# Optimization experiments

Measured on AMD Instinct MI355X. Metric: run time of the kernel, lower is better.

## Reference

```python
import jax, jax.numpy as jnp
import numpy as np
import math

EPS = 1e-7
K_NEIGHBORS = 32  # matches init kwarg k

def _project(x, c):
    norm = jnp.linalg.norm(x, axis=-1, keepdims=True).clip(EPS)
    sqrt_c = jnp.sqrt(c).clip(EPS)
    max_norm = (1.0 - EPS) / sqrt_c
    return x * jnp.minimum(max_norm / norm, 1.0)

def _mobius_add(x, y, c):
    x2 = jnp.sum(x * x, axis=-1, keepdims=True)
    y2 = jnp.sum(y * y, axis=-1, keepdims=True)
    xy = jnp.sum(x * y, axis=-1, keepdims=True)
    num = (1 + 2 * c * xy + c * y2) * x + (1 - c * x2) * y
    den = 1 + 2 * c * xy + c * c * x2 * y2
    return _project(num / den.clip(EPS), c)

def _dist(x, y, c):
    sqrt_c = jnp.sqrt(c).clip(EPS)
    diff = _mobius_add(x, -y, c)
    dn = jnp.linalg.norm(diff, axis=-1)
    arg = jnp.minimum(sqrt_c * dn.clip(EPS, 1 - EPS), 1.0 - EPS)
    return 2.0 * jnp.arctanh(arg) / sqrt_c

def _logmap0(y, c):
    sqrt_c = jnp.sqrt(c).clip(EPS)
    yn = jnp.linalg.norm(y, axis=-1, keepdims=True)
    is_zero = yn < EPS
    syn = yn.clip(EPS)
    arg = jnp.minimum(sqrt_c * syn, 1.0 - EPS)
    mag = jnp.arctanh(arg) / sqrt_c
    return jnp.where(is_zero, jnp.zeros_like(y), mag * y / syn)

def _layernorm(x, g, b):
    m = x.mean(-1, keepdims=True)
    v = x.var(-1, keepdims=True)
    return (x - m) / jnp.sqrt(v + 1e-6) * g + b

def setup_inputs() -> dict:
    key = jax.random.key(0)
    B, N, D, P, H = 2, 2048, 512, 3, 8
    ks = jax.random.split(key, 16)
    s = 0.02
    d = {}
    d['x'] = jax.random.normal(ks[0], (B, N, D), dtype=jnp.float32)
    d['positions'] = jax.random.normal(ks[1], (B, N, P), dtype=jnp.float32) * 0.1
    d['c'] = jnp.float32(1.0)
    d['Wq'] = jax.random.normal(ks[2], (D, D), jnp.float32) * s; d['bq'] = jnp.zeros((D,), jnp.float32)
    d['Wk'] = jax.random.normal(ks[3], (D, D), jnp.float32) * s; d['bk'] = jnp.zeros((D,), jnp.float32)
    d['Wv'] = jax.random.normal(ks[4], (D, D), jnp.float32) * s; d['bv'] = jnp.zeros((D,), jnp.float32)
    d['Wg'] = jax.random.normal(ks[5], (P, D), jnp.float32) * s; d['bg'] = jnp.zeros((D,), jnp.float32)
    d['Wo'] = jax.random.normal(ks[6], (D, D), jnp.float32) * s; d['bo'] = jnp.zeros((D,), jnp.float32)
    d['Wf1'] = jax.random.normal(ks[7], (D, 4 * D), jnp.float32) * s; d['bf1'] = jnp.zeros((4 * D,), jnp.float32)
    d['Wf2'] = jax.random.normal(ks[8], (4 * D, D), jnp.float32) * s; d['bf2'] = jnp.zeros((D,), jnp.float32)
    d['g1'] = jnp.ones((D,), jnp.float32); d['b1'] = jnp.zeros((D,), jnp.float32)
    d['g2'] = jnp.ones((D,), jnp.float32); d['b2'] = jnp.zeros((D,), jnp.float32)
    d['ascale'] = jnp.ones((H,), jnp.float32)
    d['fscale'] = jnp.ones((H,), jnp.float32)
    return d

def reference(x, positions, c, Wq, bq, Wk, bk, Wv, bv, Wg, bg, Wo, bo, Wf1, bf1, Wf2, bf2, g1, b1, g2, b2, ascale, fscale):
    B, N, D = x.shape
    H = ascale.shape[0]
    hd = D // H
    K = K_NEIGHBORS

    xn = _layernorm(x, g1, b1)
    q = (xn @ Wq + bq).reshape(B, N, H, hd)
    k = (xn @ Wk + bk).reshape(B, N, H, hd)
    v = (xn @ Wv + bv).reshape(B, N, H, hd)

    # full pairwise hyperbolic distance matrix [B, N, N]
    dmat = _dist(positions[:, :, None, :], positions[:, None, :, :], c)
    idx = jax.lax.top_k(-dmat, K)[1]  # [B, N, K]

    bidx = jnp.arange(B)[:, None, None]
    key_pos = positions[bidx, idx]                 # [B, N, K, P]
    qpos = positions[:, :, None, :]                # [B, N, 1, P]
    geo = _logmap0(_mobius_add(-qpos, key_pos, c), c)
    geo_v = (geo @ Wg + bg).reshape(B, N, K, H, hd)

    kg = k[bidx, idx]                              # [B, N, K, H, hd]
    vg = v[bidx, idx]

    align = jnp.einsum('bnhd,bnkhd->bhnk', q, geo_v)
    feat = jnp.einsum('bnhd,bnkhd->bhnk', q, kg) / math.sqrt(hd)
    scores = fscale[None, :, None, None] * feat + ascale[None, :, None, None] * align
    w = jax.nn.softmax(scores.astype(jnp.float32), axis=-1)
    attn = jnp.einsum('bhnk,bnkhd->bnhd', w, vg).reshape(B, N, D)

    x1 = x + attn @ Wo + bo
    h = _layernorm(x1, g2, b2)
    x2 = x1 + jax.nn.gelu(h @ Wf1 + bf1) @ Wf2 + bf2
    return x2
```

## Files before the change

### kernel.cpp

```cpp
#include <hip/hip_runtime.h>
#include <math.h>

#define EPSF 1e-7f

constexpr int Bb = 2, Nn = 2048, Dd = 512, Hh = 8, HD = 64, KK = 32;
constexpr int ROWS = Bb * Nn;

typedef __attribute__((ext_vector_type(8))) short bf16x8;
typedef __attribute__((ext_vector_type(4))) float f32x4;
typedef __attribute__((ext_vector_type(8))) unsigned short u16x8;
typedef unsigned long long u64;

__device__ inline unsigned short f2bf(float f) {
    union { float f; unsigned int u; } v; v.f = f;
    unsigned int u = v.u;
    unsigned int r = (u + 0x7fffu + ((u >> 16) & 1u)) >> 16;
    return (unsigned short)r;
}

__device__ inline float bf2f(short s) {
    union { unsigned int u; float f; } x;
    x.u = ((unsigned int)(unsigned short)s) << 16;
    return x.f;
}

__device__ inline float gelu_tanh(float v) {
    float u = v + 0.044715f * v * v * v;
    return 0.5f * v * (1.f + tanhf(0.79788456080286535588f * u));
}

__device__ __forceinline__ void tcvt(float (*tile)[65], const float* __restrict__ in,
                                     unsigned short* __restrict__ out,
                                     int K, int N, int bx, int by) {
    int k0 = by * 64, n0 = bx * 64;
    int t = threadIdx.x;
    int lr = t >> 6, lc = t & 63;
#pragma unroll 4
    for (int p = 0; p < 16; ++p) {
        int r = p * 4 + lr;
        tile[r][lc] = in[(size_t)(k0 + r) * N + n0 + lc];
    }
    __syncthreads();
#pragma unroll 4
    for (int p = 0; p < 16; ++p) {
        int n = p * 4 + lr;
        out[(size_t)(n0 + n) * K + k0 + lc] = f2bf(tile[lc][n]);
    }
}

__device__ __forceinline__ void ln_row(const float* __restrict__ x,
                                       const float* __restrict__ g,
                                       const float* __restrict__ b,
                                       unsigned short* __restrict__ out,
                                       int row, int lane) {
    const float* xr = x + (size_t)row * Dd;
    float4 v0 = *(const float4*)(xr + lane * 8);
    float4 v1 = *(const float4*)(xr + lane * 8 + 4);
    float s = v0.x + v0.y + v0.z + v0.w + v1.x + v1.y + v1.z + v1.w;
    float s2 = v0.x * v0.x + v0.y * v0.y + v0.z * v0.z + v0.w * v0.w +
               v1.x * v1.x + v1.y * v1.y + v1.z * v1.z + v1.w * v1.w;
    for (int o = 32; o; o >>= 1) { s += __shfl_xor(s, o); s2 += __shfl_xor(s2, o); }
    float mean = s * (1.f / Dd);
    float var = s2 * (1.f / Dd) - mean * mean;
    float rstd = rsqrtf(var + 1e-6f);
    float4 g0 = *(const float4*)(g + lane * 8);
    float4 g1v = *(const float4*)(g + lane * 8 + 4);
    float4 b0 = *(const float4*)(b + lane * 8);
    float4 b1v = *(const float4*)(b + lane * 8 + 4);
    u16x8 o;
    o[0] = f2bf((v0.x - mean) * rstd * g0.x + b0.x);
    o[1] = f2bf((v0.y - mean) * rstd * g0.y + b0.y);
    o[2] = f2bf((v0.z - mean) * rstd * g0.z + b0.z);
    o[3] = f2bf((v0.w - mean) * rstd * g0.w + b0.w);
    o[4] = f2bf((v1.x - mean) * rstd * g1v.x + b1v.x);
    o[5] = f2bf((v1.y - mean) * rstd * g1v.y + b1v.y);
    o[6] = f2bf((v1.z - mean) * rstd * g1v.z + b1v.z);
    o[7] = f2bf((v1.w - mean) * rstd * g1v.w + b1v.w);
    *(u16x8*)(out + (size_t)row * Dd + lane * 8) = o;
}

__global__ __launch_bounds__(256) void ln_kernel(const float* __restrict__ x,
                                                 const float* __restrict__ g,
                                                 const float* __restrict__ b,
                                                 unsigned short* __restrict__ out) {
    ln_row(x, g, b, out, blockIdx.x * 4 + (threadIdx.x >> 6), threadIdx.x & 63);
}

template <int CTRL>
__device__ inline float dpp_f(float v) {
    int i = __float_as_int(v);
    i = __builtin_amdgcn_update_dpp(i, i, CTRL, 0xF, 0xF, false);
    return __int_as_float(i);
}
template <int CTRL>
__device__ inline unsigned dpp_u(unsigned v) {
    return (unsigned)__builtin_amdgcn_update_dpp((int)v, (int)v, CTRL, 0xF, 0xF, false);
}

__device__ inline float wave_min_f32(float v) {
    v = fminf(v, dpp_f<0xB1>(v));
    v = fminf(v, dpp_f<0x4E>(v));
    v = fminf(v, dpp_f<0x141>(v));
    v = fminf(v, dpp_f<0x140>(v));
    v = fminf(v, __shfl_xor(v, 16));
    v = fminf(v, __shfl_xor(v, 32));
    return v;
}
__device__ inline unsigned wave_min_u32(unsigned v) {
    unsigned o;
    o = dpp_u<0xB1>(v);  v = o < v ? o : v;
    o = dpp_u<0x4E>(v);  v = o < v ? o : v;
    o = dpp_u<0x141>(v); v = o < v ? o : v;
    o = dpp_u<0x140>(v); v = o < v ? o : v;
    o = __shfl_xor(v, 16); v = o < v ? o : v;
    o = __shfl_xor(v, 32); v = o < v ? o : v;
    return v;
}

__device__ __forceinline__ void topk_body(char* smem, const float* __restrict__ pos,
                                          const float* __restrict__ cp,
                                          int* __restrict__ idx_out, int bid) {
    float* s_px = (float*)smem;
    float* s_py = s_px + Nn;
    float* s_pz = s_py + Nn;
    float* s_u  = s_pz + Nn;
    int* s_out  = (int*)(s_u + Nn);
    int b = bid >> 9;
    int q0 = (bid & 511) * 4;
    int t = threadIdx.x;
    float c = *cp;
    const float* pb = pos + (size_t)b * Nn * 3;
    for (int j = t; j < Nn; j += 256) {
        float px = pb[j * 3 + 0], py = pb[j * 3 + 1], pz = pb[j * 3 + 2];
        s_px[j] = px; s_py[j] = py; s_pz[j] = pz;
        s_u[j] = c * (px * px + py * py + pz * pz);
    }
    __syncthreads();
    int wave = t >> 6, lane = t & 63;
    int n = q0 + wave;
    float qx = s_px[n], qy = s_py[n], qz = s_pz[n];
    float cx2 = s_u[n];
    float x2 = cx2 / c;
    float B = 1.f - cx2;
    float rc = 1.f / c;
    float B2rc = B * B * rc;
    float m2c = -2.f * c;
    float m2B = -2.f * B;
    float key[32];
#pragma unroll
    for (int i = 0; i < 32; ++i) {
        int j = i * 64 + lane;
        float dot = qx * s_px[j] + qy * s_py[j] + qz * s_pz[j];
        float su = s_u[j];
        float r = fmaf(m2c, dot, 1.f);
        float A = r + su;
        float den = fmaf(cx2, su, r);
        float p1 = x2 * A;
        float q1 = A * dot;
        float t1 = fmaf(m2B, q1, B2rc * su);
        float num2 = fmaf(p1, A, t1);
        float rd = __builtin_amdgcn_rcpf(den);
        key[i] = fmaf(num2, rd * rd, 1.0f);
    }
    const u64 MAXK = ~0ull;
    u64 B0 = MAXK, B1 = MAXK, B2 = MAXK, B3 = MAXK;
#pragma unroll
    for (int i = 0; i < 32; ++i) {
        u64 k = ((u64)__float_as_uint(key[i]) << 32) | (unsigned int)(i * 64 + lane);
        if (k < B3) {
            B3 = k;
            if (B3 < B2) { u64 tmp = B2; B2 = B3; B3 = tmp; }
            if (B2 < B1) { u64 tmp = B1; B1 = B2; B2 = tmp; }
            if (B1 < B0) { u64 tmp = B0; B0 = B1; B1 = tmp; }
        }
    }
    int bcount = 4, consumed = 0;
    u64 last = 0;
    for (int s2 = 0; s2 < KK; ++s2) {
        bool need = (bcount == 0) && (consumed < 32);
        if (__any(need)) {
            if (need) {
                B0 = MAXK; B1 = MAXK; B2 = MAXK; B3 = MAXK;
#pragma unroll
                for (int i = 0; i < 32; ++i) {
                    u64 k = ((u64)__float_as_uint(key[i]) << 32) | (unsigned int)(i * 64 + lane);
                    if (k > last && k < B3) {
                        B3 = k;
                        if (B3 < B2) { u64 tmp = B2; B2 = B3; B3 = tmp; }
                        if (B2 < B1) { u64 tmp = B1; B1 = B2; B2 = tmp; }
                        if (B1 < B0) { u64 tmp = B0; B0 = B1; B1 = tmp; }
                    }
                }
                int rem = 32 - consumed;
                bcount = rem < 4 ? rem : 4;
            }
        }
        u64 offer = (bcount > 0) ? B0 : MAXK;
        float okey = __uint_as_float((unsigned)(offer >> 32));
        unsigned oidx = (unsigned)offer;
        float m = wave_min_f32(okey);
        u64 mask = __ballot(okey == m);
        unsigned gidx;
        if (__popcll(mask) == 1) {
            gidx = (unsigned)__shfl((int)oidx, __ffsll(mask) - 1);
        } else {
            unsigned cand = ((mask >> lane) & 1ull) ? oidx : 0xFFFFFFFFu;
            gidx = wave_min_u32(cand);
        }
        if (lane == 0) s_out[wave * KK + s2] = (int)gidx;
        if (okey == m && oidx == gidx) {
            B0 = B1; B1 = B2; B2 = B3; B3 = MAXK;
            --bcount; ++consumed;
            last = ((u64)__float_as_uint(m) << 32) | gidx;
        }
    }
    if (lane < KK) idx_out[(size_t)(b * Nn + n) * KK + lane] = s_out[wave * KK + lane];
}

__global__ __launch_bounds__(256, 4) void prep_topk_kernel(
    const float* __restrict__ Wq, const float* __restrict__ Wk,
    const float* __restrict__ Wv, const float* __restrict__ Wo,
    const float* __restrict__ Wf1, const float* __restrict__ Wf2,
    const float* __restrict__ bq, const float* __restrict__ bk, const float* __restrict__ bv,
    const float* __restrict__ x, const float* __restrict__ g1, const float* __restrict__ b1,
    unsigned short* __restrict__ wqkv_t, unsigned short* __restrict__ wo_t,
    unsigned short* __restrict__ wf1_t, unsigned short* __restrict__ wf2_t,
    float* __restrict__ bqkv, unsigned short* __restrict__ xn,
    const float* __restrict__ pos, const float* __restrict__ cp, int* __restrict__ idx_out) {
    __shared__ __align__(16) char smem[33280];
    int bid = blockIdx.x;
    if (bid >= 1798) {
        topk_body(smem, pos, cp, idx_out, bid - 1798);
        return;
    }
    float (*tile)[65] = (float (*)[65])smem;
    if (bid < 256) {
        int z = bid >> 6, r = bid & 63;
        const float* in = (z == 0) ? Wq : (z == 1) ? Wk : (z == 2) ? Wv : Wo;
        unsigned short* out = (z == 0) ? wqkv_t : (z == 1) ? wqkv_t + 262144
                            : (z == 2) ? wqkv_t + 524288 : wo_t;
        tcvt(tile, in, out, 512, 512, r & 7, r >> 3);
    } else if (bid < 512) {
        int r = bid - 256;
        tcvt(tile, Wf1, wf1_t, 512, 2048, r & 31, r >> 5);
    } else if (bid < 768) {
        int r = bid - 512;
        tcvt(tile, Wf2, wf2_t, 2048, 512, r & 7, r >> 3);
    } else if (bid < 774) {
        int t = (bid - 768) * 256 + threadIdx.x;
        if (t < 512) bqkv[t] = bq[t];
        else if (t < 1024) bqkv[t] = bk[t - 512];
        else if (t < 1536) bqkv[t] = bv[t - 1024];
    } else {
        ln_row(x, g1, b1, xn, (bid - 774) * 4 + (threadIdx.x >> 6), threadIdx.x & 63);
    }
}

template <int EPI, int OBF16>
__global__ __launch_bounds__(256) void gemm128x64(const unsigned short* __restrict__ A,
                                                  const unsigned short* __restrict__ Bt,
                                                  const float* __restrict__ bias,
                                                  const float* __restrict__ resid,
                                                  void* __restrict__ C,
                                                  int N, int K, int gridX) {
    __shared__ short As[2 * 128 * 64];
    __shared__ short Bs[2 * 64 * 64];
    int nwg = gridDim.x;
    int cpx = nwg >> 3;
    int wgid = blockIdx.x;
    int nid = (wgid & 7) * cpx + (wgid >> 3);
    int bx = nid % gridX, by = nid / gridX;
    int bm = by * 128, bn = bx * 64;
    int tid = threadIdx.x;
    int wave = tid >> 6, lane = tid & 63;
    int wr = wave >> 1, wc = wave & 1;
    f32x4 acc[4][2] = {};

    int srow = wave * 8 + (lane >> 3);
    int scol = ((lane & 7) ^ (lane >> 3)) * 8;

#define STAGE(buf, kof)                                                                                   \
    do {                                                                                                  \
        _Pragma("unroll")                                                                                 \
        for (int cc = 0; cc < 4; ++cc) {                                                                  \
            const unsigned short* ga = A + (size_t)(bm + cc * 32 + srow) * K + (kof) + scol;              \
            __builtin_amdgcn_global_load_lds((const __attribute__((address_space(1))) void*)ga,          \
                (__attribute__((address_space(3))) void*)(As + (buf) * 8192 + cc * 2048 + wave * 512),    \
                16, 0, 0);                                                                                \
        }                                                                                                 \
        _Pragma("unroll")                                                                                 \
        for (int cc = 0; cc < 2; ++cc) {                                                                  \
            const unsigned short* gb = Bt + (size_t)(bn + cc * 32 + srow) * K + (kof) + scol;             \
            __builtin_amdgcn_global_load_lds((const __attribute__((address_space(1))) void*)gb,          \
                (__attribute__((address_space(3))) void*)(Bs + (buf) * 4096 + cc * 2048 + wave * 512),    \
                16, 0, 0);                                                                                \
        }                                                                                                 \
    } while (0)

    int nt = K >> 6;
    int cur = 0;
    STAGE(0, 0);
    __syncthreads();
    for (int t = 0; t < nt; ++t) {
        if (t + 1 < nt) STAGE(cur ^ 1, (t + 1) * 64);
        const short* as = As + cur * 8192;
        const short* bs = Bs + cur * 4096;
#pragma unroll
        for (int kk = 0; kk < 64; kk += 32) {
            int kx = (kk + (lane >> 4) * 8) ^ ((lane & 7) << 3);
            bf16x8 af[4], bfr[2];
#pragma unroll
            for (int mi = 0; mi < 4; ++mi)
                af[mi] = *(const bf16x8*)(as + (wr * 64 + mi * 16 + (lane & 15)) * 64 + kx);
#pragma unroll
            for (int ni = 0; ni < 2; ++ni)
                bfr[ni] = *(const bf16x8*)(bs + (wc * 32 + ni * 16 + (lane & 15)) * 64 + kx);
#pragma unroll
            for (int mi = 0; mi < 4; ++mi)
#pragma unroll
                for (int ni = 0; ni < 2; ++ni)
                    acc[mi][ni] = __builtin_amdgcn_mfma_f32_16x16x32_bf16(af[mi], bfr[ni], acc[mi][ni], 0, 0, 0);
        }
        __syncthreads();
        cur ^= 1;
    }
#undef STAGE

    int cbase = bn + wc * 32 + (lane & 15);
    int rbase = bm + wr * 64 + (lane >> 4) * 4;
    float bias_v[2] = {bias[cbase], bias[cbase + 16]};
#pragma unroll
    for (int mi = 0; mi < 4; ++mi) {
#pragma unroll
        for (int r = 0; r < 4; ++r) {
            int row = rbase + mi * 16 + r;
#pragma unroll
            for (int ni = 0; ni < 2; ++ni) {
                int col = cbase + ni * 16;
                float v = acc[mi][ni][r] + bias_v[ni];
                if (EPI == 1) v += resid[(size_t)row * N + col];
                if (EPI == 2) v = gelu_tanh(v);
                if (OBF16) ((unsigned short*)C)[(size_t)row * N + col] = f2bf(v);
                else ((float*)C)[(size_t)row * N + col] = v;
            }
        }
    }
}

template <int EPI, int OBF16>
__global__ __launch_bounds__(256) void gemm64(const unsigned short* __restrict__ A,
                                              const unsigned short* __restrict__ Bt,
                                              const float* __restrict__ bias,
                                              const float* __restrict__ resid,
                                              void* __restrict__ C,
                                              int N, int K, int gridX) {
    __shared__ short As[2 * 64 * 64];
    __shared__ short Bs[2 * 64 * 64];
    int nwg = gridDim.x;
    int cpx = nwg >> 3;
    int wgid = blockIdx.x;
    int nid = (wgid & 7) * cpx + (wgid >> 3);
    int bx = nid % gridX, by = nid / gridX;
    int bm = by * 64, bn = bx * 64;
    int tid = threadIdx.x;
    int wave = tid >> 6, lane = tid & 63;
    int wr = wave >> 1, wc = wave & 1;
    f32x4 acc[2][2] = {};

    int srow = wave * 8 + (lane >> 3);
    int scol = ((lane & 7) ^ (lane >> 3)) * 8;
    const unsigned short* gA0 = A + (size_t)(bm + srow) * K + scol;
    const unsigned short* gA1 = A + (size_t)(bm + srow + 32) * K + scol;
    const unsigned short* gB0 = Bt + (size_t)(bn + srow) * K + scol;
    const unsigned short* gB1 = Bt + (size_t)(bn + srow + 32) * K + scol;

#define STAGE(buf, kof)                                                                                 \
    do {                                                                                                \
        __builtin_amdgcn_global_load_lds((const __attribute__((address_space(1))) void*)(gA0 + (kof)), \
            (__attribute__((address_space(3))) void*)(As + (buf) * 4096 + wave * 512), 16, 0, 0);       \
        __builtin_amdgcn_global_load_lds((const __attribute__((address_space(1))) void*)(gA1 + (kof)), \
            (__attribute__((address_space(3))) void*)(As + (buf) * 4096 + 2048 + wave * 512), 16, 0, 0);\
        __builtin_amdgcn_global_load_lds((const __attribute__((address_space(1))) void*)(gB0 + (kof)), \
            (__attribute__((address_space(3))) void*)(Bs + (buf) * 4096 + wave * 512), 16, 0, 0);       \
        __builtin_amdgcn_global_load_lds((const __attribute__((address_space(1))) void*)(gB1 + (kof)), \
            (__attribute__((address_space(3))) void*)(Bs + (buf) * 4096 + 2048 + wave * 512), 16, 0, 0);\
    } while (0)

    int nt = K >> 6;
    int cur = 0;
    STAGE(0, 0);
    __syncthreads();
    for (int t = 0; t < nt; ++t) {
        if (t + 1 < nt) STAGE(cur ^ 1, (t + 1) * 64);
        const short* as = As + cur * 4096;
        const short* bs = Bs + cur * 4096;
#pragma unroll
        for (int kk = 0; kk < 64; kk += 32) {
            int kx = (kk + (lane >> 4) * 8) ^ ((lane & 7) << 3);
            bf16x8 a0 = *(const bf16x8*)(as + (wr * 32 + (lane & 15)) * 64 + kx);
            bf16x8 a1 = *(const bf16x8*)(as + (wr * 32 + 16 + (lane & 15)) * 64 + kx);
            bf16x8 b0 = *(const bf16x8*)(bs + (wc * 32 + (lane & 15)) * 64 + kx);
            bf16x8 b1 = *(const bf16x8*)(bs + (wc * 32 + 16 + (lane & 15)) * 64 + kx);
            acc[0][0] = __builtin_amdgcn_mfma_f32_16x16x32_bf16(a0, b0, acc[0][0], 0, 0, 0);
            acc[0][1] = __builtin_amdgcn_mfma_f32_16x16x32_bf16(a0, b1, acc[0][1], 0, 0, 0);
            acc[1][0] = __builtin_amdgcn_mfma_f32_16x16x32_bf16(a1, b0, acc[1][0], 0, 0, 0);
            acc[1][1] = __builtin_amdgcn_mfma_f32_16x16x32_bf16(a1, b1, acc[1][1], 0, 0, 0);
        }
        __syncthreads();
        cur ^= 1;
    }
#undef STAGE

    int cbase = bn + wc * 32 + (lane & 15);
    int rbase = bm + wr * 32 + (lane >> 4) * 4;
    float bias_v[2] = {bias[cbase], bias[cbase + 16]};
#pragma unroll
    for (int mi = 0; mi < 2; ++mi) {
#pragma unroll
        for (int r = 0; r < 4; ++r) {
            int row = rbase + mi * 16 + r;
#pragma unroll
            for (int ni = 0; ni < 2; ++ni) {
                int col = cbase + ni * 16;
                float v = acc[mi][ni][r] + bias_v[ni];
                if (EPI == 1) v += resid[(size_t)row * N + col];
                if (EPI == 2) v = gelu_tanh(v);
                if (OBF16) ((unsigned short*)C)[(size_t)row * N + col] = f2bf(v);
                else ((float*)C)[(size_t)row * N + col] = v;
            }
        }
    }
}

__global__ __launch_bounds__(256) void attn_kernel(const unsigned short* __restrict__ qkv,
                                                   const int* __restrict__ idx,
                                                   const float* __restrict__ pos,
                                                   const float* __restrict__ Wg,
                                                   const float* __restrict__ bg,
                                                   const float* __restrict__ ascale,
                                                   const float* __restrict__ fscale,
                                                   const float* __restrict__ cp,
                                                   unsigned short* __restrict__ out) {
    constexpr int QS = 1536;
    int bid = blockIdx.x;
    int xcd = bid & 7, slot = bid >> 3;
    int b = xcd >> 2;
    int n = (xcd & 3) * 512 + slot;
    int bn = b * Nn + n;
    int t = threadIdx.x;
    int wave = t >> 6, lane = t & 63;
    __shared__ float s_q[Dd];
    __shared__ float s_geo[KK][3];
    __shared__ int s_idx[KK];
    __shared__ float s_qg[Hh][3];
    __shared__ float s_qb[Hh];
    __shared__ float s_dot[KK][9];
    __shared__ float s_w[Hh][KK];
    __shared__ float s_part[4][Dd];
    float c = *cp;
    if (t >= 64 && t < 96) s_idx[t - 64] = idx[(size_t)bn * KK + (t - 64)];
    if (t < 64) {
        bf16x8 q8 = *(const bf16x8*)(qkv + (size_t)bn * QS + t * 8);
#pragma unroll
        for (int j = 0; j < 8; ++j) s_q[t * 8 + j] = bf2f(q8[j]);
    }
    __syncthreads();
    if (t < KK) {
        const float* qp = pos + (size_t)bn * 3;
        const float* kp = pos + (size_t)(b * Nn + s_idx[t]) * 3;
        float xx = -qp[0], xyc = -qp[1], xz = -qp[2];
        float yx = kp[0], yy = kp[1], yz = kp[2];
        float x2 = xx * xx + xyc * xyc + xz * xz;
        float y2 = yx * yx + yy * yy + yz * yz;
        float xy = xx * yx + xyc * yy + xz * yz;
        float Av = 1.f + 2.f * c * xy + c * y2;
        float Bv = 1.f - c * x2;
        float den = fmaxf(1.f + 2.f * c * xy + c * c * x2 * y2, EPSF);
        float mx = (Av * xx + Bv * yx) / den;
        float my = (Av * xyc + Bv * yy) / den;
        float mz = (Av * xz + Bv * yz) / den;
        float rn = fmaxf(sqrtf(mx * mx + my * my + mz * mz), EPSF);
        float sqrt_c = fmaxf(sqrtf(c), EPSF);
        float max_norm = (1.f - EPSF) / sqrt_c;
        float scpr = fminf(max_norm / rn, 1.f);
        mx *= scpr; my *= scpr; mz *= scpr;
        float yn = sqrtf(mx * mx + my * my + mz * mz);
        if (yn < EPSF) {
            s_geo[t][0] = 0.f; s_geo[t][1] = 0.f; s_geo[t][2] = 0.f;
        } else {
            float syn = fmaxf(yn, EPSF);
            float arg = fminf(sqrt_c * syn, 1.f - EPSF);
            float mag = atanhf(arg) / sqrt_c;
            float f = mag / syn;
            s_geo[t][0] = mx * f; s_geo[t][1] = my * f; s_geo[t][2] = mz * f;
        }
    } else if (t >= 64 && t < 88) {
        int h = (t - 64) / 3, p = (t - 64) % 3;
        float acc = 0.f;
        for (int d2 = 0; d2 < HD; ++d2) acc += s_q[h * HD + d2] * Wg[p * Dd + h * HD + d2];
        s_qg[h][p] = acc;
    } else if (t >= 96 && t < 104) {
        int h = t - 96;
        float acc = 0.f;
        for (int d2 = 0; d2 < HD; ++d2) acc += s_q[h * HD + d2] * bg[h * HD + d2];
        s_qb[h] = acc;
    }
    bf16x8 v8r[8];
    {
#pragma unroll
        for (int r = 0; r < 8; ++r) {
            int kk = wave * 8 + r;
            int nk = s_idx[kk];
            bf16x8 k8 = *(const bf16x8*)(qkv + (size_t)(b * Nn + nk) * QS + 512 + lane * 8);
            float p = 0.f;
#pragma unroll
            for (int j = 0; j < 8; ++j) p = fmaf(bf2f(k8[j]), s_q[lane * 8 + j], p);
            p += __shfl_xor(p, 1);
            p += __shfl_xor(p, 2);
            p += __shfl_xor(p, 4);
            if ((lane & 7) == 0) s_dot[kk][lane >> 3] = p;
        }
#pragma unroll
        for (int r = 0; r < 8; ++r) {
            int nk = s_idx[wave * 8 + r];
            v8r[r] = *(const bf16x8*)(qkv + (size_t)(b * Nn + nk) * QS + 1024 + lane * 8);
        }
    }
    __syncthreads();
    {
        int h = t >> 5, kk = t & 31;
        float align = s_geo[kk][0] * s_qg[h][0] + s_geo[kk][1] * s_qg[h][1] +
                      s_geo[kk][2] * s_qg[h][2] + s_qb[h];
        float scv = fscale[h] * s_dot[kk][h] * 0.125f + ascale[h] * align;
        float m = scv;
        for (int o = 16; o; o >>= 1) m = fmaxf(m, __shfl_xor(m, o));
        float e = expf(scv - m);
        float ss = e;
        for (int o = 16; o; o >>= 1) ss += __shfl_xor(ss, o);
        s_w[h][kk] = e / ss;
    }
    __syncthreads();
    {
        float acc[8] = {0.f, 0.f, 0.f, 0.f, 0.f, 0.f, 0.f, 0.f};
        int h = lane >> 3;
#pragma unroll
        for (int r = 0; r < 8; ++r) {
            float wgt = s_w[h][wave * 8 + r];
#pragma unroll
            for (int j = 0; j < 8; ++j) acc[j] = fmaf(bf2f(v8r[r][j]), wgt, acc[j]);
        }
#pragma unroll
        for (int j = 0; j < 8; ++j) s_part[wave][lane * 8 + j] = acc[j];
    }
    __syncthreads();
    for (int d = t; d < Dd; d += 256) {
        float s = s_part[0][d] + s_part[1][d] + s_part[2][d] + s_part[3][d];
        out[(size_t)bn * Dd + d] = f2bf(s);
    }
}

extern "C" void kernel_launch(void* const* d_in, const int* in_sizes, int n_in,
                              void* d_out, int out_size, void* d_ws, size_t ws_size,
                              hipStream_t stream) {
    const float* x   = (const float*)d_in[0];
    const float* pos = (const float*)d_in[1];
    const float* cp  = (const float*)d_in[2];
    const float* Wq  = (const float*)d_in[3];
    const float* bq  = (const float*)d_in[4];
    const float* Wk  = (const float*)d_in[5];
    const float* bk  = (const float*)d_in[6];
    const float* Wv  = (const float*)d_in[7];
    const float* bv  = (const float*)d_in[8];
    const float* Wg  = (const float*)d_in[9];
    const float* bg  = (const float*)d_in[10];
    const float* Wo  = (const float*)d_in[11];
    const float* bo  = (const float*)d_in[12];
    const float* Wf1 = (const float*)d_in[13];
    const float* bf1 = (const float*)d_in[14];
    const float* Wf2 = (const float*)d_in[15];
    const float* bf2 = (const float*)d_in[16];
    const float* g1  = (const float*)d_in[17];
    const float* b1  = (const float*)d_in[18];
    const float* g2  = (const float*)d_in[19];
    const float* b2  = (const float*)d_in[20];
    const float* asc = (const float*)d_in[21];
    const float* fsc = (const float*)d_in[22];
    float* out = (float*)d_out;
    char* ws = (char*)d_ws;

    unsigned short* qkv_bf  = (unsigned short*)(ws + 0);
    unsigned short* t_bf    = (unsigned short*)(ws + 0);
    unsigned short* xn_bf   = (unsigned short*)(ws + 25165824);
    float*          x1      = (float*)(ws + 29360128);
    unsigned short* attn_bf = (unsigned short*)(ws + 37748736);
    unsigned short* wqkv_t  = (unsigned short*)(ws + 41943040);
    unsigned short* wo_t    = (unsigned short*)(ws + 43515904);
    unsigned short* wf1_t   = (unsigned short*)(ws + 44040192);
    unsigned short* wf2_t   = (unsigned short*)(ws + 46137344);
    int*            idx     = (int*)(ws + 48234496);
    float*          bqkv    = (float*)(ws + 48758784);

    prep_topk_kernel<<<1798 + 1024, 256, 0, stream>>>(
        Wq, Wk, Wv, Wo, Wf1, Wf2, bq, bk, bv, x, g1, b1,
        wqkv_t, wo_t, wf1_t, wf2_t, bqkv, xn_bf, pos, cp, idx);
    gemm128x64<0, 1><<<768, 256, 0, stream>>>(xn_bf, wqkv_t, bqkv, nullptr, qkv_bf, 1536, 512, 24);
    attn_kernel<<<ROWS, 256, 0, stream>>>(qkv_bf, idx, pos, Wg, bg, asc, fsc, cp, attn_bf);
    gemm64<1, 0><<<512, 256, 0, stream>>>(attn_bf, wo_t, bo, x, x1, 512, 512, 8);
    ln_kernel<<<ROWS / 4, 256, 0, stream>>>(x1, g2, b2, xn_bf);
    gemm128x64<2, 1><<<1024, 256, 0, stream>>>(xn_bf, wf1_t, bf1, nullptr, t_bf, 2048, 512, 32);
    gemm64<1, 0><<<512, 256, 0, stream>>>(t_bf, wf2_t, bf2, x1, out, 512, 2048, 8);
}
```

Before: 134.3 us.

## Process one query row per wavefront in attention, removing shared memory and barriers

```diff
diff --git a/kernel.cpp b/kernel.cpp
--- a/kernel.cpp
+++ b/kernel.cpp
@@ -445,29 +445,23 @@
     int bid = blockIdx.x;
     int xcd = bid & 7, slot = bid >> 3;
     int b = xcd >> 2;
-    int n = (xcd & 3) * 512 + slot;
+    int wave = threadIdx.x >> 6, lane = threadIdx.x & 63;
+    int n = (xcd & 3) * 512 + slot * 4 + wave;
     int bn = b * Nn + n;
-    int t = threadIdx.x;
-    int wave = t >> 6, lane = t & 63;
-    __shared__ float s_q[Dd];
-    __shared__ float s_geo[KK][3];
-    __shared__ int s_idx[KK];
-    __shared__ float s_qg[Hh][3];
-    __shared__ float s_qb[Hh];
-    __shared__ float s_dot[KK][9];
-    __shared__ float s_w[Hh][KK];
-    __shared__ float s_part[4][Dd];
     float c = *cp;
-    if (t >= 64 && t < 96) s_idx[t - 64] = idx[(size_t)bn * KK + (t - 64)];
-    if (t < 64) {
-        bf16x8 q8 = *(const bf16x8*)(qkv + (size_t)bn * QS + t * 8);
-#pragma unroll
-        for (int j = 0; j < 8; ++j) s_q[t * 8 + j] = bf2f(q8[j]);
-    }
-    __syncthreads();
-    if (t < KK) {
+    int h = lane >> 3;
+
+    bf16x8 q8 = *(const bf16x8*)(qkv + (size_t)bn * QS + lane * 8);
+    float qf[8];
+#pragma unroll
+    for (int j = 0; j < 8; ++j) qf[j] = bf2f(q8[j]);
+
+    int myidx = idx[(size_t)bn * KK + (lane & 31)];
+
+    float gx, gy, gz;
+    {
         const float* qp = pos + (size_t)bn * 3;
-        const float* kp = pos + (size_t)(b * Nn + s_idx[t]) * 3;
+        const float* kp = pos + (size_t)(b * Nn + myidx) * 3;
         float xx = -qp[0], xyc = -qp[1], xz = -qp[2];
         float yx = kp[0], yy = kp[1], yz = kp[2];
         float x2 = xx * xx + xyc * xyc + xz * xz;
@@ -486,77 +480,71 @@
         mx *= scpr; my *= scpr; mz *= scpr;
         float yn = sqrtf(mx * mx + my * my + mz * mz);
         if (yn < EPSF) {
-            s_geo[t][0] = 0.f; s_geo[t][1] = 0.f; s_geo[t][2] = 0.f;
+            gx = 0.f; gy = 0.f; gz = 0.f;
         } else {
             float syn = fmaxf(yn, EPSF);
             float arg = fminf(sqrt_c * syn, 1.f - EPSF);
             float mag = atanhf(arg) / sqrt_c;
             float f = mag / syn;
-            s_geo[t][0] = mx * f; s_geo[t][1] = my * f; s_geo[t][2] = mz * f;
-        }
-    } else if (t >= 64 && t < 88) {
-        int h = (t - 64) / 3, p = (t - 64) % 3;
-        float acc = 0.f;
-        for (int d2 = 0; d2 < HD; ++d2) acc += s_q[h * HD + d2] * Wg[p * Dd + h * HD + d2];
-        s_qg[h][p] = acc;
-    } else if (t >= 96 && t < 104) {
-        int h = t - 96;
-        float acc = 0.f;
-        for (int d2 = 0; d2 < HD; ++d2) acc += s_q[h * HD + d2] * bg[h * HD + d2];
-        s_qb[h] = acc;
-    }
-    bf16x8 v8r[8];
-    {
-#pragma unroll
-        for (int r = 0; r < 8; ++r) {
-            int kk = wave * 8 + r;
-            int nk = s_idx[kk];
-            bf16x8 k8 = *(const bf16x8*)(qkv + (size_t)(b * Nn + nk) * QS + 512 + lane * 8);
-            float p = 0.f;
-#pragma unroll
-            for (int j = 0; j < 8; ++j) p = fmaf(bf2f(k8[j]), s_q[lane * 8 + j], p);
-            p += __shfl_xor(p, 1);
-            p += __shfl_xor(p, 2);
-            p += __shfl_xor(p, 4);
-            if ((lane & 7) == 0) s_dot[kk][lane >> 3] = p;
-        }
-#pragma unroll
-        for (int r = 0; r < 8; ++r) {
-            int nk = s_idx[wave * 8 + r];
-            v8r[r] = *(const bf16x8*)(qkv + (size_t)(b * Nn + nk) * QS + 1024 + lane * 8);
-        }
-    }
-    __syncthreads();
-    {
-        int h = t >> 5, kk = t & 31;
-        float align = s_geo[kk][0] * s_qg[h][0] + s_geo[kk][1] * s_qg[h][1] +
-                      s_geo[kk][2] * s_qg[h][2] + s_qb[h];
-        float scv = fscale[h] * s_dot[kk][h] * 0.125f + ascale[h] * align;
-        float m = scv;
-        for (int o = 16; o; o >>= 1) m = fmaxf(m, __shfl_xor(m, o));
-        float e = expf(scv - m);
-        float ss = e;
-        for (int o = 16; o; o >>= 1) ss += __shfl_xor(ss, o);
-        s_w[h][kk] = e / ss;
-    }
-    __syncthreads();
-    {
-        float acc[8] = {0.f, 0.f, 0.f, 0.f, 0.f, 0.f, 0.f, 0.f};
-        int h = lane >> 3;
-#pragma unroll
-        for (int r = 0; r < 8; ++r) {
-            float wgt = s_w[h][wave * 8 + r];
-#pragma unroll
-            for (int j = 0; j < 8; ++j) acc[j] = fmaf(bf2f(v8r[r][j]), wgt, acc[j]);
-        }
-#pragma unroll
-        for (int j = 0; j < 8; ++j) s_part[wave][lane * 8 + j] = acc[j];
-    }
-    __syncthreads();
-    for (int d = t; d < Dd; d += 256) {
-        float s = s_part[0][d] + s_part[1][d] + s_part[2][d] + s_part[3][d];
-        out[(size_t)bn * Dd + d] = f2bf(s);
-    }
+            gx = mx * f; gy = my * f; gz = mz * f;
+        }
+    }
+
+    float qg0 = 0.f, qg1 = 0.f, qg2 = 0.f, qbv = 0.f;
+#pragma unroll
+    for (int j = 0; j < 8; ++j) {
+        int d = lane * 8 + j;
+        qg0 = fmaf(qf[j], Wg[d], qg0);
+        qg1 = fmaf(qf[j], Wg[512 + d], qg1);
+        qg2 = fmaf(qf[j], Wg[1024 + d], qg2);
+        qbv = fmaf(qf[j], bg[d], qbv);
+    }
+#pragma unroll
+    for (int o = 1; o < 8; o <<= 1) {
+        qg0 += __shfl_xor(qg0, o);
+        qg1 += __shfl_xor(qg1, o);
+        qg2 += __shfl_xor(qg2, o);
+        qbv += __shfl_xor(qbv, o);
+    }
+
+    float fs = fscale[h] * 0.125f;
+    float as = ascale[h];
+
+    float scv[32];
+#pragma unroll
+    for (int r = 0; r < 32; ++r) {
+        int nk = __shfl(myidx, r);
+        bf16x8 k8 = *(const bf16x8*)(qkv + (size_t)(b * Nn + nk) * QS + 512 + lane * 8);
+        float p = 0.f;
+#pragma unroll
+        for (int j = 0; j < 8; ++j) p = fmaf(bf2f(k8[j]), qf[j], p);
+        p += __shfl_xor(p, 1);
+        p += __shfl_xor(p, 2);
+        p += __shfl_xor(p, 4);
+        float gxr = __shfl(gx, r), gyr = __shfl(gy, r), gzr = __shfl(gz, r);
+        float align = fmaf(gxr, qg0, fmaf(gyr, qg1, fmaf(gzr, qg2, qbv)));
+        scv[r] = fmaf(fs, p, as * align);
+    }
+    float m = scv[0];
+#pragma unroll
+    for (int r = 1; r < 32; ++r) m = fmaxf(m, scv[r]);
+
+    float acc[8] = {0.f, 0.f, 0.f, 0.f, 0.f, 0.f, 0.f, 0.f};
+    float ss = 0.f;
+#pragma unroll
+    for (int r = 0; r < 32; ++r) {
+        int nk = __shfl(myidx, r);
+        bf16x8 v8 = *(const bf16x8*)(qkv + (size_t)(b * Nn + nk) * QS + 1024 + lane * 8);
+        float e = expf(scv[r] - m);
+        ss += e;
+#pragma unroll
+        for (int j = 0; j < 8; ++j) acc[j] = fmaf(bf2f(v8[j]), e, acc[j]);
+    }
+    float rs = 1.f / ss;
+    u16x8 o;
+#pragma unroll
+    for (int j = 0; j < 8; ++j) o[j] = f2bf(acc[j] * rs);
+    *(u16x8*)(out + (size_t)bn * Dd + lane * 8) = o;
 }
 
 extern "C" void kernel_launch(void* const* d_in, const int* in_sizes, int n_in,
@@ -604,7 +592,7 @@
         Wq, Wk, Wv, Wo, Wf1, Wf2, bq, bk, bv, x, g1, b1,
         wqkv_t, wo_t, wf1_t, wf2_t, bqkv, xn_bf, pos, cp, idx);
     gemm128x64<0, 1><<<768, 256, 0, stream>>>(xn_bf, wqkv_t, bqkv, nullptr, qkv_bf, 1536, 512, 24);
-    attn_kernel<<<ROWS, 256, 0, stream>>>(qkv_bf, idx, pos, Wg, bg, asc, fsc, cp, attn_bf);
+    attn_kernel<<<ROWS / 4, 256, 0, stream>>>(qkv_bf, idx, pos, Wg, bg, asc, fsc, cp, attn_bf);
     gemm64<1, 0><<<512, 256, 0, stream>>>(attn_bf, wo_t, bo, x, x1, 512, 512, 8);
     ln_kernel<<<ROWS / 4, 256, 0, stream>>>(x1, g2, b2, xn_bf);
     gemm128x64<2, 1><<<1024, 256, 0, stream>>>(xn_bf, wf1_t, bf1, nullptr, t_bf, 2048, 512, 32);
```

Result: slower. 146.8 us (+9.3%).
